# Optimization experiments

Measured on AMD Instinct MI355X. Metric: run time of the kernel, lower is better.

The kernel has to match this reference:

```python
import jax, jax.numpy as jnp
import numpy as np

N = 2048          # nodes
IN_DIM = 512      # in_dim
H = 8             # num_heads
HD = IN_DIM // H  # head_dim = 64
L = 5             # max_path_len
E = 32768         # edges
D_EDGE = 64       # edge_feat_dim


def setup_inputs() -> dict:
    key = jax.random.key(0)
    ks = jax.random.split(key, 14)
    w = 1.0 / np.sqrt(IN_DIM)
    return {
        "node_feat": jax.random.normal(ks[0], (N, IN_DIM), jnp.float32),
        "edge_index": jax.random.randint(ks[1], (2, E), 0, N, dtype=jnp.int32),
        "max_path_len": 5,
        "shortest_distances": jax.random.randint(ks[2], (N, N), 0, L + 1, dtype=jnp.int32),
        "shortest_paths": jax.random.randint(ks[3], (N, N, L), 0, E + 1, dtype=jnp.int32),  # E == padding row
        "edge_feat": jax.random.normal(ks[4], (E, D_EDGE), jnp.float32),
        "attention_mask": jnp.zeros((N, N), jnp.int32),
        "WQ": jax.random.normal(ks[5], (IN_DIM, IN_DIM), jnp.float32) * w,
        "bQ": jax.random.normal(ks[6], (IN_DIM,), jnp.float32) * 0.02,
        "WK": jax.random.normal(ks[7], (IN_DIM, IN_DIM), jnp.float32) * w,
        "bK": jax.random.normal(ks[8], (IN_DIM,), jnp.float32) * 0.02,
        "WV": jax.random.normal(ks[9], (IN_DIM, IN_DIM), jnp.float32) * w,
        "bV": jax.random.normal(ks[10], (IN_DIM,), jnp.float32) * 0.02,
        "WO": jax.random.normal(ks[11], (IN_DIM, IN_DIM), jnp.float32) * w,
        "bO": jnp.zeros((IN_DIM,), jnp.float32),
        "spatial_bias": jax.random.normal(ks[12], ((L + 1) * H, 1), jnp.float32) * 0.02,
        "edge_weight": jax.random.normal(ks[13], ((L + 1) * H, D_EDGE), jnp.float32) * 0.02,
    }


def reference(node_feat, edge_index, max_path_len, shortest_distances, shortest_paths,
              edge_feat, attention_mask, WQ, bQ, WK, bK, WV, bV, WO, bO,
              spatial_bias, edge_weight):
    Nn, D = node_feat.shape
    Lp = max_path_len  # min(max_path_len, max_shortest_path_len); distances reach Lp here

    Q = (node_feat @ WQ + bQ).reshape(Nn, H, HD)
    K = (node_feat @ WK + bK).reshape(Nn, H, HD)
    V = (node_feat @ WV + bV).reshape(Nn, H, HD)

    # QK^T / sqrt(head_dim), laid out [N, N, H] as in the original after permute
    scores = jnp.einsum('nhd,mhd->nmh', Q, K) / np.sqrt(HD).astype(np.float32)

    # SpatialEncoding: bias table [(L+1)*H, 1] -> [L+1, H]; gather by clamped distance
    sp_table = spatial_bias.reshape(Lp + 1, H)
    dist = jnp.clip(shortest_distances, 0, Lp)
    scores = scores + sp_table[dist]  # [N, N, H]

    # EdgeEncoding: einsum('xyld,ldh->xyh') refactored as per-edge projection then gather
    W_e = edge_weight[: Lp * H].reshape(Lp, H, D_EDGE)  # (reshape[L,H,D].permute -> [L,D,H])
    padded = jnp.concatenate([edge_feat, jnp.zeros((1, D_EDGE), edge_feat.dtype)], axis=0)
    T = jnp.einsum('ed,lhd->elh', padded, W_e)  # [E+1, L, H]
    sp = shortest_paths[:, :, :Lp]
    gathered = T[sp, jnp.arange(Lp)[None, None, :]]  # [N, N, L, H]
    scores = scores + gathered.sum(axis=2)

    mask = attention_mask.astype(bool)
    scores = jnp.where(mask[:, :, None], -jnp.inf, scores)

    # NOTE: original applies softmax over dim=-1 of the [N, N, H] tensor (the head axis);
    # faithfully reproduced here. Dropout is identity (eval / p for inference).
    attn = jax.nn.softmax(scores, axis=-1)

    out = jnp.einsum('nmh,mhd->nhd', attn, V).reshape(Nn, D)
    return out @ WO + bO
```

## Files before the change

kernel.cpp:

```cpp
#include <hip/hip_runtime.h>

#define NN     2048
#define DIM    512
#define NH     8
#define HD     64
#define NE     32768
#define EPAD   32832
#define CHUNKS 4
#define CHSZ   (NN/CHUNKS)
#define NJT    (CHSZ/64)
#define LOG2E  1.4426950408889634f

typedef __attribute__((ext_vector_type(8))) short bf16x8;
typedef __attribute__((ext_vector_type(4))) float f32x4;
typedef __attribute__((ext_vector_type(4))) unsigned int u32x4;

#define MFMA(a,b,c) __builtin_amdgcn_mfma_f32_16x16x32_bf16((a),(b),(c),0,0,0)

__device__ __forceinline__ float bf2f(unsigned int u16){
  union { unsigned int i; float f; } v; v.i = u16 << 16; return v.f;
}
__device__ __forceinline__ unsigned short f2bf(float f){
  union { float ff; unsigned int i; } v; v.ff = f;
  return (unsigned short)((v.i + 0x7fffu + ((v.i >> 16) & 1u)) >> 16);
}

__global__ __launch_bounds__(256) void cvt_k(
    const float* __restrict__ X, const float* __restrict__ ef, const float* __restrict__ ew,
    unsigned short* __restrict__ Xb, unsigned short* __restrict__ pEF, unsigned short* __restrict__ pEW)
{
  long g = (long)blockIdx.x*256 + threadIdx.x;
  const long GX = (long)NN*DIM/8;
  const long GE = (long)EPAD*8;
  const float* src; unsigned short* dst; long off, lim8;
  if (g < GX){ src = X;  dst = Xb;  off = g;        lim8 = GX; }
  else if (g < GX+GE){ src = ef; dst = pEF; off = g-GX; lim8 = (long)NE*8; }
  else { off = g-GX-GE; if (off >= 512) return; src = ew; dst = pEW; lim8 = 320; }
  unsigned short o[8];
  if (off < lim8){
    #pragma unroll
    for (int i=0;i<8;i++) o[i] = f2bf(src[off*8+i]);
  } else {
    #pragma unroll
    for (int i=0;i<8;i++) o[i] = 0;
  }
  *(uint4*)(dst + off*8) = *(const uint4*)o;
}

__global__ __launch_bounds__(256) void transpose512(
    const float* __restrict__ a0, const float* __restrict__ a1,
    const float* __restrict__ a2, const float* __restrict__ a3,
    unsigned short* __restrict__ out)
{
  __shared__ unsigned short tile[32][33];
  const float* src = blockIdx.z==0 ? a0 : blockIdx.z==1 ? a1 : blockIdx.z==2 ? a2 : a3;
  unsigned short* dst = out + (size_t)blockIdx.z*DIM*DIM;
  int bx = blockIdx.x*32, by = blockIdx.y*32;
  int tx = threadIdx.x, ty = threadIdx.y;
  #pragma unroll
  for (int i=0;i<32;i+=8) tile[ty+i][tx] = f2bf(src[(size_t)(by+ty+i)*DIM + bx+tx]);
  __syncthreads();
  #pragma unroll
  for (int i=0;i<32;i+=8) dst[(size_t)(bx+ty+i)*DIM + by+tx] = tile[tx][ty+i];
}

__global__ __launch_bounds__(256) void gemm_bt(
    const unsigned short* __restrict__ A1, const unsigned short* __restrict__ A2,
    const float* __restrict__ bias, unsigned short* __restrict__ C, float* __restrict__ Cf,
    int M, int N, int K, int bias_row)
{
  int lane = threadIdx.x & 63, w = threadIdx.x >> 6;
  int quad = lane >> 4, low = lane & 15;
  int m0 = blockIdx.y*64 + w*16;
  int n0 = blockIdx.x*32;
  f32x4 acc[2];
  acc[0] = (f32x4){0.f,0.f,0.f,0.f};
  acc[1] = (f32x4){0.f,0.f,0.f,0.f};
  for (int k0=0; k0<K; k0+=32){
    bf16x8 a = *(const bf16x8*)(A1 + (size_t)(m0+low)*K + k0 + quad*8);
    #pragma unroll
    for (int t=0;t<2;t++){
      bf16x8 b = *(const bf16x8*)(A2 + (size_t)(n0+16*t+low)*K + k0 + quad*8);
      acc[t] = MFMA(a, b, acc[t]);
    }
  }
  #pragma unroll
  for (int t=0;t<2;t++){
    #pragma unroll
    for (int r=0;r<4;r++){
      int row = m0 + quad*4 + r;
      int col = n0 + 16*t + low;
      float v = acc[t][r];
      if (bias) v += bias[bias_row ? row : col];
      if (Cf) Cf[(size_t)row*N + col] = v;
      else    C [(size_t)row*N + col] = f2bf(v);
    }
  }
}

__global__ __launch_bounds__(256) void bias_k(
    const unsigned short* __restrict__ T2, const float* __restrict__ spb,
    const int* __restrict__ dist, const int* __restrict__ sp, const int* __restrict__ maskp,
    unsigned short* __restrict__ biasB)
{
  __shared__ float sptab[48];
  if (threadIdx.x < 48) sptab[threadIdx.x] = spb[threadIdx.x];
  __syncthreads();
  long pix = (long)blockIdx.x*256 + threadIdx.x;
  int dd = __builtin_nontemporal_load(dist + pix);
  int mk = __builtin_nontemporal_load(maskp + pix);
  int e[5];
  #pragma unroll
  for (int l=0;l<5;l++) e[l] = __builtin_nontemporal_load(sp + pix*5 + l);
  dd = dd < 0 ? 0 : (dd > 5 ? 5 : dd);
  float b[8];
  #pragma unroll
  for (int x=0;x<8;x++) b[x] = sptab[dd*8 + x];
  #pragma unroll
  for (int l=0;l<5;l++){
    int ee = e[l];
    if ((unsigned)ee > (unsigned)NE) ee = NE;
    uint4 tv = *(const uint4*)(T2 + (size_t)ee*64 + l*8);
    b[0] += bf2f(tv.x & 0xffffu); b[1] += bf2f(tv.x >> 16);
    b[2] += bf2f(tv.y & 0xffffu); b[3] += bf2f(tv.y >> 16);
    b[4] += bf2f(tv.z & 0xffffu); b[5] += bf2f(tv.z >> 16);
    b[6] += bf2f(tv.w & 0xffffu); b[7] += bf2f(tv.w >> 16);
  }
  unsigned short o[8];
  #pragma unroll
  for (int x=0;x<8;x++) o[x] = mk ? f2bf(-1e30f) : f2bf(b[x]);
  u32x4 ov = *(const u32x4*)o;
  __builtin_nontemporal_store(ov, (u32x4*)(biasB + pix*8));
}

__global__ __launch_bounds__(512) void attn_k(
    const unsigned short* __restrict__ Qb, const unsigned short* __restrict__ Kb,
    const unsigned short* __restrict__ Vt, const unsigned short* __restrict__ biasB,
    float* __restrict__ partO)
{
  __shared__ __attribute__((aligned(16))) float sld[NH][16][68];
  int tid = threadIdx.x;
  int lane = tid & 63, h = tid >> 6;
  int quad = lane >> 4, low = lane & 15;
  int q0 = blockIdx.x * 16;
  int chunk = blockIdx.y;

  bf16x8 aq[2];
  #pragma unroll
  for (int s=0;s<2;s++)
    aq[s] = *(const bf16x8*)(Qb + (size_t)(q0+low)*DIM + h*HD + s*32 + quad*8);

  f32x4 accO[4];
  #pragma unroll
  for (int t=0;t<4;t++) accO[t] = (f32x4){0.f,0.f,0.f,0.f};

  uint4 pb[2];
  #pragma unroll
  for (int it=0; it<2; ++it){
    int p = tid + it*512;
    int qq = p >> 6, mm = p & 63;
    pb[it] = *(const uint4*)(biasB + ((size_t)(q0+qq)*NN + chunk*CHSZ + mm)*8);
  }

  for (int jt=0; jt<NJT; ++jt){
    int m0 = chunk*CHSZ + jt*64;
    __syncthreads();

    #pragma unroll
    for (int it=0; it<2; ++it){
      int p = tid + it*512;
      int qq = p >> 6, mm = p & 63;
      uint4 tv = pb[it];
      sld[0][qq][mm] = bf2f(tv.x & 0xffffu); sld[1][qq][mm] = bf2f(tv.x >> 16);
      sld[2][qq][mm] = bf2f(tv.y & 0xffffu); sld[3][qq][mm] = bf2f(tv.y >> 16);
      sld[4][qq][mm] = bf2f(tv.z & 0xffffu); sld[5][qq][mm] = bf2f(tv.z >> 16);
      sld[6][qq][mm] = bf2f(tv.w & 0xffffu); sld[7][qq][mm] = bf2f(tv.w >> 16);
    }
    if (jt+1 < NJT){
      #pragma unroll
      for (int it=0; it<2; ++it){
        int p = tid + it*512;
        int qq = p >> 6, mm = p & 63;
        pb[it] = *(const uint4*)(biasB + ((size_t)(q0+qq)*NN + m0 + 64 + mm)*8);
      }
    }
    __syncthreads();

    f32x4 S[4];
    #pragma unroll
    for (int t=0;t<4;t++) S[t] = (f32x4){0.f,0.f,0.f,0.f};
    #pragma unroll
    for (int s=0;s<2;s++){
      #pragma unroll
      for (int t=0;t<4;t++){
        bf16x8 bk = *(const bf16x8*)(Kb + (size_t)(m0+16*t+low)*DIM + h*HD + s*32 + quad*8);
        S[t] = MFMA(aq[s], bk, S[t]);
      }
    }
    #pragma unroll
    for (int t=0;t<4;t++){
      #pragma unroll
      for (int r=0;r<4;r++){
        float* slot = &sld[h][quad*4+r][low+16*t];
        *slot = S[t][r]*0.125f + *slot;
      }
    }
    __syncthreads();

    #pragma unroll
    for (int it=0; it<2; ++it){
      int p = tid + it*512;
      int qq = p >> 6, mm = p & 63;
      float s0[8];
      #pragma unroll
      for (int x=0;x<8;x++) s0[x] = sld[x][qq][mm];
      float mx = s0[0];
      #pragma unroll
      for (int x=1;x<8;x++) mx = fmaxf(mx, s0[x]);
      float sum = 0.f;
      #pragma unroll
      for (int x=0;x<8;x++){ s0[x] = exp2f((s0[x]-mx)*LOG2E); sum += s0[x]; }
      float inv = (mx < -1e29f) ? 0.f : 1.f/sum;
      #pragma unroll
      for (int x=0;x<8;x++) sld[x][qq][mm] = s0[x]*inv;
    }
    __syncthreads();

    bf16x8 ap[2];
    #pragma unroll
    for (int s=0;s<2;s++){
      const float* pp = &sld[h][low][s*32 + quad*8];
      float4 x0 = *(const float4*)pp;
      float4 x1 = *(const float4*)(pp + 4);
      bf16x8 a;
      a[0]=(short)f2bf(x0.x); a[1]=(short)f2bf(x0.y); a[2]=(short)f2bf(x0.z); a[3]=(short)f2bf(x0.w);
      a[4]=(short)f2bf(x1.x); a[5]=(short)f2bf(x1.y); a[6]=(short)f2bf(x1.z); a[7]=(short)f2bf(x1.w);
      ap[s] = a;
    }
    #pragma unroll
    for (int s=0;s<2;s++){
      #pragma unroll
      for (int t=0;t<4;t++){
        bf16x8 bv = *(const bf16x8*)(Vt + (size_t)(h*HD + 16*t + low)*NN + m0 + s*32 + quad*8);
        accO[t] = MFMA(ap[s], bv, accO[t]);
      }
    }
  }

  #pragma unroll
  for (int t=0;t<4;t++){
    #pragma unroll
    for (int r=0;r<4;r++){
      int q = quad*4 + r;
      partO[(((size_t)chunk*NN + q0 + q)*NH + h)*HD + 16*t + low] = accO[t][r];
    }
  }
}

__global__ __launch_bounds__(512) void merge_k(const float* __restrict__ partO,
                                               unsigned short* __restrict__ Obf)
{
  size_t idx = (size_t)blockIdx.x*512 + threadIdx.x;
  float s = 0.f;
  #pragma unroll
  for (int c=0;c<CHUNKS;c++) s += partO[(size_t)c*NN*DIM + idx];
  Obf[idx] = f2bf(s);
}

extern "C" void kernel_launch(void* const* d_in, const int* in_sizes, int n_in,
                              void* d_out, int out_size, void* d_ws, size_t ws_size,
                              hipStream_t stream)
{
  const float* X    = (const float*)d_in[0];
  const int*  dist  = (const int*)d_in[3];
  const int*  sp    = (const int*)d_in[4];
  const float* ef   = (const float*)d_in[5];
  const int*  maskp = (const int*)d_in[6];
  const float* WQ   = (const float*)d_in[7];
  const float* bQ   = (const float*)d_in[8];
  const float* WK   = (const float*)d_in[9];
  const float* bK   = (const float*)d_in[10];
  const float* WV   = (const float*)d_in[11];
  const float* bV   = (const float*)d_in[12];
  const float* WO   = (const float*)d_in[13];
  const float* bO   = (const float*)d_in[14];
  const float* spb  = (const float*)d_in[15];
  const float* ew   = (const float*)d_in[16];

  char* ws = (char*)d_ws;
  unsigned short* Wt   = (unsigned short*)(ws + 0);
  unsigned short* Xb   = (unsigned short*)(ws + 2097152);
  unsigned short* Qb   = (unsigned short*)(ws + 4194304);
  unsigned short* Kb   = (unsigned short*)(ws + 6291456);
  unsigned short* Vtb  = (unsigned short*)(ws + 8388608);
  unsigned short* pEF  = (unsigned short*)(ws + 10485760);
  unsigned short* pEW  = (unsigned short*)(ws + 14688256);
  unsigned short* T2   = (unsigned short*)(ws + 14696448);
  unsigned short* Obf  = (unsigned short*)(ws + 18898944);
  unsigned short* biasB= (unsigned short*)(ws + 20996096);
  float*          pO   = (float*)(ws + 88104960);

  cvt_k<<<dim3(1540), dim3(256), 0, stream>>>(X, ef, ew, Xb, pEF, pEW);
  transpose512<<<dim3(16,16,4), dim3(32,8), 0, stream>>>(WQ, WK, WV, WO, Wt);
  gemm_bt<<<dim3(2,513),  dim3(256), 0, stream>>>(pEF, pEW, (const float*)nullptr, T2, (float*)nullptr, EPAD, 64, 64, 0);
  bias_k<<<dim3(NN*NN/256), dim3(256), 0, stream>>>(T2, spb, dist, sp, maskp, biasB);
  gemm_bt<<<dim3(16,32),  dim3(256), 0, stream>>>(Xb,  Wt,          bQ, Qb,  (float*)nullptr, NN, DIM, DIM, 0);
  gemm_bt<<<dim3(16,32),  dim3(256), 0, stream>>>(Xb,  Wt + 262144, bK, Kb,  (float*)nullptr, NN, DIM, DIM, 0);
  gemm_bt<<<dim3(64,8),   dim3(256), 0, stream>>>(Wt + 524288, Xb,  bV, Vtb, (float*)nullptr, DIM, NN, DIM, 1);
  attn_k<<<dim3(128,CHUNKS), dim3(512), 0, stream>>>(Qb, Kb, Vtb, biasB, pO);
  merge_k<<<dim3(2048), dim3(512), 0, stream>>>(pO, Obf);
  gemm_bt<<<dim3(16,32), dim3(256), 0, stream>>>(Obf, Wt + 786432, bO, (unsigned short*)nullptr, (float*)d_out, NN, DIM, DIM, 0);
}
```

Before: 426.9 us.

## Fuse QKV projections and relayout edge table per path level for bias gather

Merges the three Q/K/V projection GEMMs into one kernel that reuses each X fragment across all three weight matrices, with V written transposed directly. The edge-projection table is stored level-major ([L][E][8]), so each path-level gather in the bias kernel reads a dense 32 MB/5 sub-table, which should improve cache locality. It also adds unrolling to the generic GEMM K loop and replaces the nontemporal bias store with a normal store. The risks are higher register pressure in the fused QKV kernel and scattered 2-byte writes in the new T2 layout.

Result: faster. 397.5 us (-6.9%).

```diff
diff --git a/kernel.cpp b/kernel.cpp
--- a/kernel.cpp
+++ b/kernel.cpp
@@ -76,6 +76,7 @@
   f32x4 acc[2];
   acc[0] = (f32x4){0.f,0.f,0.f,0.f};
   acc[1] = (f32x4){0.f,0.f,0.f,0.f};
+  #pragma unroll 4
   for (int k0=0; k0<K; k0+=32){
     bf16x8 a = *(const bf16x8*)(A1 + (size_t)(m0+low)*K + k0 + quad*8);
     #pragma unroll
@@ -98,8 +99,76 @@
   }
 }
 
+__global__ __launch_bounds__(256) void gemm_t2(
+    const unsigned short* __restrict__ A1, const unsigned short* __restrict__ A2,
+    unsigned short* __restrict__ T2L)
+{
+  int lane = threadIdx.x & 63, w = threadIdx.x >> 6;
+  int quad = lane >> 4, low = lane & 15;
+  int m0 = blockIdx.y*64 + w*16;
+  int n0 = blockIdx.x*32;
+  f32x4 acc[2];
+  acc[0] = (f32x4){0.f,0.f,0.f,0.f};
+  acc[1] = (f32x4){0.f,0.f,0.f,0.f};
+  #pragma unroll
+  for (int k0=0; k0<64; k0+=32){
+    bf16x8 a = *(const bf16x8*)(A1 + (size_t)(m0+low)*64 + k0 + quad*8);
+    #pragma unroll
+    for (int t=0;t<2;t++){
+      bf16x8 b = *(const bf16x8*)(A2 + (size_t)(n0+16*t+low)*64 + k0 + quad*8);
+      acc[t] = MFMA(a, b, acc[t]);
+    }
+  }
+  #pragma unroll
+  for (int t=0;t<2;t++){
+    #pragma unroll
+    for (int r=0;r<4;r++){
+      int row = m0 + quad*4 + r;
+      int col = n0 + 16*t + low;
+      T2L[((size_t)(col>>3)*EPAD + row)*8 + (col&7)] = f2bf(acc[t][r]);
+    }
+  }
+}
+
+__global__ __launch_bounds__(256) void qkv_k(
+    const unsigned short* __restrict__ Xb, const unsigned short* __restrict__ Wt,
+    const float* __restrict__ bQ, const float* __restrict__ bK, const float* __restrict__ bV,
+    unsigned short* __restrict__ Qb, unsigned short* __restrict__ Kb, unsigned short* __restrict__ Vtb)
+{
+  int lane = threadIdx.x & 63, w = threadIdx.x >> 6;
+  int quad = lane >> 4, low = lane & 15;
+  int m0 = blockIdx.y*64 + w*16;
+  int n0 = blockIdx.x*32;
+  f32x4 acc[3][2];
+  #pragma unroll
+  for (int z=0;z<3;z++){ acc[z][0]=(f32x4){0.f,0.f,0.f,0.f}; acc[z][1]=(f32x4){0.f,0.f,0.f,0.f}; }
+  #pragma unroll 2
+  for (int k0=0; k0<DIM; k0+=32){
+    bf16x8 a = *(const bf16x8*)(Xb + (size_t)(m0+low)*DIM + k0 + quad*8);
+    #pragma unroll
+    for (int z=0;z<3;z++){
+      #pragma unroll
+      for (int t=0;t<2;t++){
+        bf16x8 b = *(const bf16x8*)(Wt + (size_t)z*DIM*DIM + (size_t)(n0+16*t+low)*DIM + k0 + quad*8);
+        acc[z][t] = MFMA(a, b, acc[z][t]);
+      }
+    }
+  }
+  #pragma unroll
+  for (int t=0;t<2;t++){
+    #pragma unroll
+    for (int r=0;r<4;r++){
+      int row = m0 + quad*4 + r;
+      int col = n0 + 16*t + low;
+      Qb[(size_t)row*DIM + col] = f2bf(acc[0][t][r] + bQ[col]);
+      Kb[(size_t)row*DIM + col] = f2bf(acc[1][t][r] + bK[col]);
+      Vtb[(size_t)col*NN + row] = f2bf(acc[2][t][r] + bV[col]);
+    }
+  }
+}
+
 __global__ __launch_bounds__(256) void bias_k(
-    const unsigned short* __restrict__ T2, const float* __restrict__ spb,
+    const unsigned short* __restrict__ T2L, const float* __restrict__ spb,
     const int* __restrict__ dist, const int* __restrict__ sp, const int* __restrict__ maskp,
     unsigned short* __restrict__ biasB)
 {
@@ -120,7 +189,7 @@
   for (int l=0;l<5;l++){
     int ee = e[l];
     if ((unsigned)ee > (unsigned)NE) ee = NE;
-    uint4 tv = *(const uint4*)(T2 + (size_t)ee*64 + l*8);
+    uint4 tv = *(const uint4*)(T2L + ((size_t)l*EPAD + ee)*8);
     b[0] += bf2f(tv.x & 0xffffu); b[1] += bf2f(tv.x >> 16);
     b[2] += bf2f(tv.y & 0xffffu); b[3] += bf2f(tv.y >> 16);
     b[4] += bf2f(tv.z & 0xffffu); b[5] += bf2f(tv.z >> 16);
@@ -129,8 +198,7 @@
   unsigned short o[8];
   #pragma unroll
   for (int x=0;x<8;x++) o[x] = mk ? f2bf(-1e30f) : f2bf(b[x]);
-  u32x4 ov = *(const u32x4*)o;
-  __builtin_nontemporal_store(ov, (u32x4*)(biasB + pix*8));
+  *(uint4*)(biasB + pix*8) = *(const uint4*)o;
 }
 
 __global__ __launch_bounds__(512) void attn_k(
@@ -295,18 +363,16 @@
   unsigned short* Vtb  = (unsigned short*)(ws + 8388608);
   unsigned short* pEF  = (unsigned short*)(ws + 10485760);
   unsigned short* pEW  = (unsigned short*)(ws + 14688256);
-  unsigned short* T2   = (unsigned short*)(ws + 14696448);
+  unsigned short* T2L  = (unsigned short*)(ws + 14696448);
   unsigned short* Obf  = (unsigned short*)(ws + 18898944);
   unsigned short* biasB= (unsigned short*)(ws + 20996096);
   float*          pO   = (float*)(ws + 88104960);
 
   cvt_k<<<dim3(1540), dim3(256), 0, stream>>>(X, ef, ew, Xb, pEF, pEW);
   transpose512<<<dim3(16,16,4), dim3(32,8), 0, stream>>>(WQ, WK, WV, WO, Wt);
-  gemm_bt<<<dim3(2,513),  dim3(256), 0, stream>>>(pEF, pEW, (const float*)nullptr, T2, (float*)nullptr, EPAD, 64, 64, 0);
-  bias_k<<<dim3(NN*NN/256), dim3(256), 0, stream>>>(T2, spb, dist, sp, maskp, biasB);
-  gemm_bt<<<dim3(16,32),  dim3(256), 0, stream>>>(Xb,  Wt,          bQ, Qb,  (float*)nullptr, NN, DIM, DIM, 0);
-  gemm_bt<<<dim3(16,32),  dim3(256), 0, stream>>>(Xb,  Wt + 262144, bK, Kb,  (float*)nullptr, NN, DIM, DIM, 0);
-  gemm_bt<<<dim3(64,8),   dim3(256), 0, stream>>>(Wt + 524288, Xb,  bV, Vtb, (float*)nullptr, DIM, NN, DIM, 1);
+  gemm_t2<<<dim3(2,513), dim3(256), 0, stream>>>(pEF, pEW, T2L);
+  bias_k<<<dim3(NN*NN/256), dim3(256), 0, stream>>>(T2L, spb, dist, sp, maskp, biasB);
+  qkv_k<<<dim3(16,32), dim3(256), 0, stream>>>(Xb, Wt, bQ, bK, bV, Qb, Kb, Vtb);
   attn_k<<<dim3(128,CHUNKS), dim3(512), 0, stream>>>(Qb, Kb, Vtb, biasB, pO);
   merge_k<<<dim3(2048), dim3(512), 0, stream>>>(pO, Obf);
   gemm_bt<<<dim3(16,32), dim3(256), 0, stream>>>(Obf, Wt + 786432, bO, (unsigned short*)nullptr, (float*)d_out, NN, DIM, DIM, 0);
```
